# Optimization experiments

Measured on AMD Instinct MI355X. Metric: run time of the kernel, lower is better.

## Reference

```python
import jax, jax.numpy as jnp
import numpy as np

NUM_ITERATIONS = 3
SOFTMAX_DIM = 1  # softmax over out_capsules


def _squash(x, axis=-1):
    # scale = ||x|| / (1 + ||x||^2)  (leftthomas/CapsuleLayer squash)
    norm = jnp.linalg.norm(x, axis=axis, keepdims=True)
    return x * (norm / (1.0 + norm * norm))


def _normalize(x, axis=-1, eps=1e-12):
    n = jnp.linalg.norm(x, axis=axis, keepdims=True)
    return x / jnp.maximum(n, eps)


def setup_inputs() -> dict:
    key = jax.random.key(0)
    k1, k2, k3 = jax.random.split(key, 3)
    B, I, O, LIN, LOUT = 64, 512, 64, 8, 16
    x = jax.random.normal(k1, (B, I, LIN), dtype=jnp.float32)
    # xavier-uniform over last two dims of the 4D weight
    limit = float(np.sqrt(6.0 / (LIN + LOUT)))
    weight = jax.random.uniform(k2, (O, I, LOUT, LIN), jnp.float32, -limit, limit)
    blim = float(np.sqrt(6.0 / (O + LOUT)))
    bias = jax.random.uniform(k3, (O, LOUT), jnp.float32, -blim, blim)
    return {"x": x, "weight": weight, "bias": bias}


def reference(x, weight, bias):
    # priors[b,o,i,v] = sum_l weight[o,i,v,l] * x[b,i,l]  -> [B, O, I, Lout]
    priors = jnp.einsum('oivl,bil->boiv', weight, x)
    # k-means routing, 'dot' similarity
    out = jnp.mean(priors, axis=-2, keepdims=True)  # [B, O, 1, Lout]
    for _ in range(NUM_ITERATIONS):
        logits = jnp.sum(priors * _normalize(out, axis=-1), axis=-1, keepdims=True)  # [B,O,I,1]
        probs = jax.nn.softmax(logits, axis=SOFTMAX_DIM)  # over out_capsules
        out = jnp.sum(probs * priors, axis=-2, keepdims=True)  # [B,O,1,Lout]
    out = _squash(out, axis=-1).squeeze(-2)  # [B, O, Lout]
    return out + bias
```

## Files before the change

kernel.cpp:

```cpp
#include <hip/hip_runtime.h>
#include <hip/hip_bf16.h>
#include <cstdint>


typedef float float4v __attribute__((ext_vector_type(4)));
typedef float float2v __attribute__((ext_vector_type(2)));
typedef unsigned short ushort8 __attribute__((ext_vector_type(8)));

__device__ __forceinline__ float bf2f(unsigned short u) {
    union { unsigned int ui; float f; } cv;
    cv.ui = ((unsigned int)u) << 16;
    return cv.f;
}
__device__ __forceinline__ unsigned short f2bf(float f) {
    union { float f; unsigned int ui; } cv;
    cv.f = f;
    unsigned int u = cv.ui;
    unsigned int r = u + 0x7FFFu + ((u >> 16) & 1u);
    return (unsigned short)(r >> 16);
}

__global__ __launch_bounds__(256) void k_priors(const float* __restrict__ W,
                                                const float* __restrict__ x,
                                                unsigned short* __restrict__ priors,
                                                float* __restrict__ outb) {
    const int i = blockIdx.x;
    const int t = threadIdx.x;
    __shared__ float Wl[16 * 132];
    __shared__ float xl[512];

    {
        int j = (blockIdx.x * 256 + t) * 2;
        *(float2v*)(outb + j) = (float2v){0.0f, 0.0f};
    }

    if (t < 128) {
        float4v v = *(const float4v*)(x + ((size_t)(t >> 1) * 512 + i) * 8 + (size_t)(t & 1) * 4);
        *(float4v*)(xl + t * 4) = v;
    }

    const int r  = t & 15;
    const int bq = t >> 4;

    for (int oc = 0; oc < 4; ++oc) {
        __syncthreads();
        #pragma unroll
        for (int k = 0; k < 2; ++k) {
            int j  = t + k * 256;
            int ol = j >> 5;
            int r4 = j & 31;
            float4v v = *(const float4v*)(W + ((size_t)((oc * 16 + ol) * 512 + i)) * 128 + (size_t)r4 * 4);
            *(float4v*)(Wl + ol * 132 + r4 * 4) = v;
        }
        __syncthreads();

        float4v wreg[32];
        const float4v* wp = (const float4v*)(Wl + r * 132);
        #pragma unroll
        for (int j = 0; j < 32; ++j) wreg[j] = wp[j];

        const int o = oc * 16 + r;
        #pragma unroll
        for (int k = 0; k < 4; ++k) {
            const int b = bq + 16 * k;
            float4v xr0 = ((const float4v*)(xl + b * 8))[0];
            float4v xr1 = ((const float4v*)(xl + b * 8))[1];
            ushort8 u0, u1;
            #pragma unroll
            for (int v = 0; v < 16; ++v) {
                float s = 0.0f;
                #pragma unroll
                for (int l = 0; l < 8; ++l) {
                    int idx = v * 8 + l;
                    float wv = wreg[idx >> 2][idx & 3];
                    float xv = (l < 4) ? xr0[l & 3] : xr1[l & 3];
                    s = fmaf(wv, xv, s);
                }
                unsigned short hb = f2bf(s);
                if (v < 8) u0[v] = hb; else u1[v - 8] = hb;
            }
            unsigned short* dst = priors + ((size_t)(b * 512 + i) * 64 + o) * 16;
            *(ushort8*)(dst) = u0;
            *(ushort8*)(dst + 8) = u1;
        }
    }
}

__global__ __launch_bounds__(256) void k_sum0(const unsigned short* __restrict__ priors,
                                              float* __restrict__ out0) {
    const int b    = blockIdx.x >> 3;
    const int ic   = blockIdx.x & 7;
    const int t    = threadIdx.x;
    const int slot = t & 127;
    const int io   = t >> 7;
    const int o    = slot >> 1;
    const int vh   = slot & 1;

    float acc[8];
    #pragma unroll
    for (int j = 0; j < 8; ++j) acc[j] = 0.0f;

    const unsigned short* base = priors + (size_t)b * 524288 + (size_t)o * 16 + vh * 8;
    for (int k = 0; k < 32; ++k) {
        const int i = ic * 64 + k * 2 + io;
        ushort8 u = *(const ushort8*)(base + (size_t)i * 1024);
        #pragma unroll
        for (int j = 0; j < 8; ++j) acc[j] += bf2f(u[j]);
    }

    __shared__ float red[8 * 128];
    if (io == 1) {
        #pragma unroll
        for (int j = 0; j < 8; ++j) red[j * 128 + slot] = acc[j];
    }
    __syncthreads();
    if (io == 0) {
        float* dst = out0 + (size_t)b * 1024 + o * 16 + vh * 8;
        #pragma unroll
        for (int j = 0; j < 8; ++j) atomicAdd(dst + j, acc[j] + red[j * 128 + slot]);
    }
}

__global__ __launch_bounds__(256) void k_route(const unsigned short* __restrict__ priors,
                                               const float* __restrict__ out_prev,
                                               float* __restrict__ out_next) {
    const int b    = blockIdx.x >> 3;
    const int h    = blockIdx.x & 7;
    const int t    = threadIdx.x;
    const int w    = t >> 6;
    const int lane = t & 63;

    __shared__ float noutT[16 * 64];
    __shared__ float accbuf[4 * 1088];

    if (t < 64) {
        const float* po = out_prev + (size_t)b * 1024 + t * 16;
        float vv[16]; float n2 = 0.0f;
        #pragma unroll
        for (int j = 0; j < 16; ++j) { vv[j] = po[j]; n2 += vv[j] * vv[j]; }
        float n = fmaxf(sqrtf(n2), 1e-12f);
        float inv = 1.0f / n;
        #pragma unroll
        for (int j = 0; j < 16; ++j) noutT[j * 64 + t] = vv[j] * inv;
    }
    __syncthreads();

    float nr[16];
    #pragma unroll
    for (int j = 0; j < 16; ++j) nr[j] = noutT[j * 64 + lane];

    float acc[16];
    #pragma unroll
    for (int j = 0; j < 16; ++j) acc[j] = 0.0f;

    const size_t base = (size_t)b * 524288 + (size_t)lane * 16;
    for (int k = 0; k < 16; ++k) {
        const int i = h * 64 + w + 4 * k;
        const ushort8* pp = (const ushort8*)(priors + base + (size_t)i * 1024);
        ushort8 u0 = pp[0], u1 = pp[1];
        float pf[16];
        #pragma unroll
        for (int j = 0; j < 8; ++j) { pf[j] = bf2f(u0[j]); pf[8 + j] = bf2f(u1[j]); }

        float logit = 0.0f;
        #pragma unroll
        for (int j = 0; j < 16; ++j) logit = fmaf(pf[j], nr[j], logit);

        float m = logit;
        #pragma unroll
        for (int d = 1; d < 64; d <<= 1) m = fmaxf(m, __shfl_xor(m, d));
        float e = __expf(logit - m);
        float s = e;
        #pragma unroll
        for (int d = 1; d < 64; d <<= 1) s += __shfl_xor(s, d);
        float p = e / s;

        #pragma unroll
        for (int j = 0; j < 16; ++j) acc[j] = fmaf(p, pf[j], acc[j]);
    }

    #pragma unroll
    for (int j = 0; j < 16; ++j) accbuf[w * 1088 + lane * 17 + j] = acc[j];
    __syncthreads();

    for (int j = t; j < 1024; j += 256) {
        const int o = j >> 4, v = j & 15;
        const int idx = o * 17 + v;
        float s = accbuf[idx] + accbuf[1088 + idx] + accbuf[2176 + idx] + accbuf[3264 + idx];
        atomicAdd(out_next + (size_t)b * 1024 + j, s);
    }
}

__global__ __launch_bounds__(64) void k_fin(const float* __restrict__ outl,
                                            const float* __restrict__ bias,
                                            float* __restrict__ out) {
    const int b = blockIdx.x;
    const int o = threadIdx.x;
    const float* p = outl + (size_t)b * 1024 + o * 16;
    float vv[16]; float n2 = 0.0f;
    #pragma unroll
    for (int j = 0; j < 16; ++j) { vv[j] = p[j]; n2 += vv[j] * vv[j]; }
    float n = sqrtf(n2);
    float scale = n / (1.0f + n2);
    float* q = out + (size_t)b * 1024 + o * 16;
    #pragma unroll
    for (int j = 0; j < 16; ++j) q[j] = vv[j] * scale + bias[o * 16 + j];
}

extern "C" void kernel_launch(void* const* d_in, const int* in_sizes, int n_in,
                              void* d_out, int out_size, void* d_ws, size_t ws_size,
                              hipStream_t stream) {
    const float* x    = (const float*)d_in[0];
    const float* W    = (const float*)d_in[1];
    const float* bias = (const float*)d_in[2];
    float* out = (float*)d_out;

    unsigned short* priors = (unsigned short*)d_ws;
    float* outb = (float*)((char*)d_ws + (size_t)64 * 512 * 64 * 16 * 2);

    k_priors<<<512, 256, 0, stream>>>(W, x, priors, outb);
    k_sum0  <<<512, 256, 0, stream>>>(priors, outb);
    k_route <<<512, 256, 0, stream>>>(priors, outb,               outb + 65536);
    k_route <<<512, 256, 0, stream>>>(priors, outb + 65536,       outb + 2 * 65536);
    k_route <<<512, 256, 0, stream>>>(priors, outb + 2 * 65536,   outb + 3 * 65536);
    k_fin   <<<64, 64, 0, stream>>>(outb + 3 * 65536, bias, out);
}
```

Baseline: 99.74 us.

## Fuse sum and routing iterations into one cooperative kernel with register-resident priors

Replaces the sum0, three route and finalize kernels with a single cooperative-launch kernel of 256 blocks x 512 threads. Each thread loads its slice of bf16 priors into registers once and reuses it across all routing iterations, separated by grid-wide syncs. This removes four launches and three re-reads of the 64 MB priors buffer. In exchange it adds grid barrier cost and heavy register pressure (256 bytes of cached priors per thread), with a fallback to the old kernels if the cooperative launch fails.

```diff
diff --git a/kernel.cpp b/kernel.cpp
--- a/kernel.cpp
+++ b/kernel.cpp
@@ -1,5 +1,6 @@
 #include <hip/hip_runtime.h>
 #include <hip/hip_bf16.h>
+#include <hip/hip_cooperative_groups.h>
 #include <cstdint>
 
 
@@ -86,6 +87,137 @@
     }
 }
 
+__global__ __launch_bounds__(512, 2) void k_fused(const unsigned short* __restrict__ priors,
+                                                  float* __restrict__ outb,
+                                                  const float* __restrict__ bias,
+                                                  float* __restrict__ out) {
+    const int b    = blockIdx.x >> 2;
+    const int q    = blockIdx.x & 3;
+    const int t    = threadIdx.x;
+    const int w    = t >> 6;
+    const int lane = t & 63;
+
+    __shared__ float noutT[16 * 64];
+    __shared__ float red[7 * 1088];
+
+    ushort8 c0[16], c1[16];
+    float acc[16];
+    #pragma unroll
+    for (int j = 0; j < 16; ++j) acc[j] = 0.0f;
+
+    const unsigned short* basep = priors + (size_t)b * 524288
+                                + (size_t)(q * 128 + w * 16) * 1024 + (size_t)lane * 16;
+    #pragma unroll
+    for (int k = 0; k < 16; ++k) {
+        c0[k] = *(const ushort8*)(basep + (size_t)k * 1024);
+        c1[k] = *(const ushort8*)(basep + (size_t)k * 1024 + 8);
+        #pragma unroll
+        for (int j = 0; j < 8; ++j) {
+            acc[j]     += bf2f(c0[k][j]);
+            acc[8 + j] += bf2f(c1[k][j]);
+        }
+    }
+    if (w > 0) {
+        #pragma unroll
+        for (int j = 0; j < 16; ++j) red[(w - 1) * 1088 + lane * 17 + j] = acc[j];
+    }
+    __syncthreads();
+    if (w == 0) {
+        float* dst = outb + (size_t)b * 1024 + lane * 16;
+        #pragma unroll
+        for (int j = 0; j < 16; ++j) {
+            float s = acc[j];
+            #pragma unroll
+            for (int ww = 0; ww < 7; ++ww) s += red[ww * 1088 + lane * 17 + j];
+            atomicAdd(dst + j, s);
+        }
+    }
+
+    cooperative_groups::this_grid().sync();
+
+    for (int r = 0; r < 3; ++r) {
+        const float* oprev = outb + (size_t)r * 65536 + (size_t)b * 1024;
+        float*       onext = outb + (size_t)(r + 1) * 65536 + (size_t)b * 1024;
+
+        if (t < 64) {
+            float vv[16]; float n2 = 0.0f;
+            #pragma unroll
+            for (int j = 0; j < 16; ++j) {
+                vv[j] = __hip_atomic_load(oprev + t * 16 + j, __ATOMIC_RELAXED,
+                                          __HIP_MEMORY_SCOPE_AGENT);
+                n2 += vv[j] * vv[j];
+            }
+            float inv = 1.0f / fmaxf(sqrtf(n2), 1e-12f);
+            #pragma unroll
+            for (int j = 0; j < 16; ++j) noutT[j * 64 + t] = vv[j] * inv;
+        }
+        __syncthreads();
+
+        float nr[16];
+        #pragma unroll
+        for (int j = 0; j < 16; ++j) nr[j] = noutT[j * 64 + lane];
+
+        float a2[16];
+        #pragma unroll
+        for (int j = 0; j < 16; ++j) a2[j] = 0.0f;
+
+        #pragma unroll
+        for (int k = 0; k < 16; ++k) {
+            float pf[16];
+            #pragma unroll
+            for (int j = 0; j < 8; ++j) { pf[j] = bf2f(c0[k][j]); pf[8 + j] = bf2f(c1[k][j]); }
+
+            float logit = 0.0f;
+            #pragma unroll
+            for (int j = 0; j < 16; ++j) logit = fmaf(pf[j], nr[j], logit);
+
+            float m = logit;
+            #pragma unroll
+            for (int d = 1; d < 64; d <<= 1) m = fmaxf(m, __shfl_xor(m, d));
+            float e = __expf(logit - m);
+            float s = e;
+            #pragma unroll
+            for (int d = 1; d < 64; d <<= 1) s += __shfl_xor(s, d);
+            float p = e / s;
+
+            #pragma unroll
+            for (int j = 0; j < 16; ++j) a2[j] = fmaf(p, pf[j], a2[j]);
+        }
+
+        __syncthreads();
+        if (w > 0) {
+            #pragma unroll
+            for (int j = 0; j < 16; ++j) red[(w - 1) * 1088 + lane * 17 + j] = a2[j];
+        }
+        __syncthreads();
+        if (w == 0) {
+            #pragma unroll
+            for (int j = 0; j < 16; ++j) {
+                float s = a2[j];
+                #pragma unroll
+                for (int ww = 0; ww < 7; ++ww) s += red[ww * 1088 + lane * 17 + j];
+                atomicAdd(onext + lane * 16 + j, s);
+            }
+        }
+        cooperative_groups::this_grid().sync();
+    }
+
+    if (q == 0 && t < 64) {
+        const float* p = outb + (size_t)3 * 65536 + (size_t)b * 1024 + t * 16;
+        float vv[16]; float n2 = 0.0f;
+        #pragma unroll
+        for (int j = 0; j < 16; ++j) {
+            vv[j] = __hip_atomic_load(p + j, __ATOMIC_RELAXED, __HIP_MEMORY_SCOPE_AGENT);
+            n2 += vv[j] * vv[j];
+        }
+        float n = sqrtf(n2);
+        float sc = n / (1.0f + n2);
+        float* qd = out + (size_t)b * 1024 + t * 16;
+        #pragma unroll
+        for (int j = 0; j < 16; ++j) qd[j] = vv[j] * sc + bias[t * 16 + j];
+    }
+}
+
 __global__ __launch_bounds__(256) void k_sum0(const unsigned short* __restrict__ priors,
                                               float* __restrict__ out0) {
     const int b    = blockIdx.x >> 3;
@@ -138,8 +270,7 @@
         float vv[16]; float n2 = 0.0f;
         #pragma unroll
         for (int j = 0; j < 16; ++j) { vv[j] = po[j]; n2 += vv[j] * vv[j]; }
-        float n = fmaxf(sqrtf(n2), 1e-12f);
-        float inv = 1.0f / n;
+        float inv = 1.0f / fmaxf(sqrtf(n2), 1e-12f);
         #pragma unroll
         for (int j = 0; j < 16; ++j) noutT[j * 64 + t] = vv[j] * inv;
     }
@@ -219,9 +350,16 @@
     float* outb = (float*)((char*)d_ws + (size_t)64 * 512 * 64 * 16 * 2);
 
     k_priors<<<512, 256, 0, stream>>>(W, x, priors, outb);
-    k_sum0  <<<512, 256, 0, stream>>>(priors, outb);
-    k_route <<<512, 256, 0, stream>>>(priors, outb,               outb + 65536);
-    k_route <<<512, 256, 0, stream>>>(priors, outb + 65536,       outb + 2 * 65536);
-    k_route <<<512, 256, 0, stream>>>(priors, outb + 2 * 65536,   outb + 3 * 65536);
-    k_fin   <<<64, 64, 0, stream>>>(outb + 3 * 65536, bias, out);
-}
+
+    void* args[] = { (void*)&priors, (void*)&outb, (void*)&bias, (void*)&out };
+    hipError_t err = hipLaunchCooperativeKernel((const void*)k_fused, dim3(256), dim3(512),
+                                                args, 0, stream);
+    if (err != hipSuccess) {
+        (void)hipGetLastError();
+        k_sum0  <<<512, 256, 0, stream>>>(priors, outb);
+        k_route <<<512, 256, 0, stream>>>(priors, outb,               outb + 65536);
+        k_route <<<512, 256, 0, stream>>>(priors, outb + 65536,       outb + 2 * 65536);
+        k_route <<<512, 256, 0, stream>>>(priors, outb + 2 * 65536,   outb + 3 * 65536);
+        k_fin   <<<64, 64, 0, stream>>>(outb + 3 * 65536, bias, out);
+    }
+}
```

Measured after the change: 276.5 us. +177.2%, slower.

## Replace atomic accumulation with per-chunk partial buffers and double grid size

Applied to the files above, without the earlier changes.

The routing and sum kernels now write per-chunk partial sums into a [B,16,1024] buffer instead of doing float atomicAdds into a shared output. The consumer kernels (next route step and final squash) reduce the 16 partials themselves. Each kernel launch also doubles its block count, with each block covering half as many input capsules, to raise parallelism. This removes the atomics and the zero-initialisation done inside k_priors, at the cost of extra partial-buffer traffic and a redundant 16-way reduction in every block.

```diff
diff --git a/kernel.cpp b/kernel.cpp
--- a/kernel.cpp
+++ b/kernel.cpp
@@ -4,7 +4,6 @@
 
 
 typedef float float4v __attribute__((ext_vector_type(4)));
-typedef float float2v __attribute__((ext_vector_type(2)));
 typedef unsigned short ushort8 __attribute__((ext_vector_type(8)));
 
 __device__ __forceinline__ float bf2f(unsigned short u) {
@@ -22,17 +21,11 @@
 
 __global__ __launch_bounds__(256) void k_priors(const float* __restrict__ W,
                                                 const float* __restrict__ x,
-                                                unsigned short* __restrict__ priors,
-                                                float* __restrict__ outb) {
+                                                unsigned short* __restrict__ priors) {
     const int i = blockIdx.x;
     const int t = threadIdx.x;
     __shared__ float Wl[16 * 132];
     __shared__ float xl[512];
-
-    {
-        int j = (blockIdx.x * 256 + t) * 2;
-        *(float2v*)(outb + j) = (float2v){0.0f, 0.0f};
-    }
 
     if (t < 128) {
         float4v v = *(const float4v*)(x + ((size_t)(t >> 1) * 512 + i) * 8 + (size_t)(t & 1) * 4);
@@ -87,9 +80,9 @@
 }
 
 __global__ __launch_bounds__(256) void k_sum0(const unsigned short* __restrict__ priors,
-                                              float* __restrict__ out0) {
-    const int b    = blockIdx.x >> 3;
-    const int ic   = blockIdx.x & 7;
+                                              float* __restrict__ part0) {
+    const int b    = blockIdx.x >> 4;
+    const int ic   = blockIdx.x & 15;
     const int t    = threadIdx.x;
     const int slot = t & 127;
     const int io   = t >> 7;
@@ -101,8 +94,9 @@
     for (int j = 0; j < 8; ++j) acc[j] = 0.0f;
 
     const unsigned short* base = priors + (size_t)b * 524288 + (size_t)o * 16 + vh * 8;
-    for (int k = 0; k < 32; ++k) {
-        const int i = ic * 64 + k * 2 + io;
+    #pragma unroll
+    for (int k = 0; k < 16; ++k) {
+        const int i = ic * 32 + k * 2 + io;
         ushort8 u = *(const ushort8*)(base + (size_t)i * 1024);
         #pragma unroll
         for (int j = 0; j < 8; ++j) acc[j] += bf2f(u[j]);
@@ -115,17 +109,17 @@
     }
     __syncthreads();
     if (io == 0) {
-        float* dst = out0 + (size_t)b * 1024 + o * 16 + vh * 8;
-        #pragma unroll
-        for (int j = 0; j < 8; ++j) atomicAdd(dst + j, acc[j] + red[j * 128 + slot]);
+        float* dst = part0 + (size_t)b * 16384 + (size_t)ic * 1024 + o * 16 + vh * 8;
+        #pragma unroll
+        for (int j = 0; j < 8; ++j) dst[j] = acc[j] + red[j * 128 + slot];
     }
 }
 
 __global__ __launch_bounds__(256) void k_route(const unsigned short* __restrict__ priors,
-                                               const float* __restrict__ out_prev,
-                                               float* __restrict__ out_next) {
-    const int b    = blockIdx.x >> 3;
-    const int h    = blockIdx.x & 7;
+                                               const float* __restrict__ part_prev,
+                                               float* __restrict__ part_next) {
+    const int b    = blockIdx.x >> 4;
+    const int h    = blockIdx.x & 15;
     const int t    = threadIdx.x;
     const int w    = t >> 6;
     const int lane = t & 63;
@@ -134,12 +128,20 @@
     __shared__ float accbuf[4 * 1088];
 
     if (t < 64) {
-        const float* po = out_prev + (size_t)b * 1024 + t * 16;
+        const float* pp = part_prev + (size_t)b * 16384 + t * 16;
+        float4v s4[4];
+        #pragma unroll
+        for (int g = 0; g < 4; ++g) s4[g] = (float4v){0.f, 0.f, 0.f, 0.f};
+        #pragma unroll
+        for (int ic = 0; ic < 16; ++ic) {
+            #pragma unroll
+            for (int g = 0; g < 4; ++g)
+                s4[g] += *(const float4v*)(pp + (size_t)ic * 1024 + g * 4);
+        }
         float vv[16]; float n2 = 0.0f;
         #pragma unroll
-        for (int j = 0; j < 16; ++j) { vv[j] = po[j]; n2 += vv[j] * vv[j]; }
-        float n = fmaxf(sqrtf(n2), 1e-12f);
-        float inv = 1.0f / n;
+        for (int j = 0; j < 16; ++j) { vv[j] = s4[j >> 2][j & 3]; n2 += vv[j] * vv[j]; }
+        float inv = 1.0f / fmaxf(sqrtf(n2), 1e-12f);
         #pragma unroll
         for (int j = 0; j < 16; ++j) noutT[j * 64 + t] = vv[j] * inv;
     }
@@ -154,8 +156,9 @@
     for (int j = 0; j < 16; ++j) acc[j] = 0.0f;
 
     const size_t base = (size_t)b * 524288 + (size_t)lane * 16;
-    for (int k = 0; k < 16; ++k) {
-        const int i = h * 64 + w + 4 * k;
+    #pragma unroll
+    for (int k = 0; k < 8; ++k) {
+        const int i = h * 32 + w + 4 * k;
         const ushort8* pp = (const ushort8*)(priors + base + (size_t)i * 1024);
         ushort8 u0 = pp[0], u1 = pp[1];
         float pf[16];
@@ -183,23 +186,32 @@
     for (int j = 0; j < 16; ++j) accbuf[w * 1088 + lane * 17 + j] = acc[j];
     __syncthreads();
 
+    float* dst = part_next + (size_t)b * 16384 + (size_t)h * 1024;
     for (int j = t; j < 1024; j += 256) {
         const int o = j >> 4, v = j & 15;
         const int idx = o * 17 + v;
-        float s = accbuf[idx] + accbuf[1088 + idx] + accbuf[2176 + idx] + accbuf[3264 + idx];
-        atomicAdd(out_next + (size_t)b * 1024 + j, s);
-    }
-}
-
-__global__ __launch_bounds__(64) void k_fin(const float* __restrict__ outl,
+        dst[j] = accbuf[idx] + accbuf[1088 + idx] + accbuf[2176 + idx] + accbuf[3264 + idx];
+    }
+}
+
+__global__ __launch_bounds__(64) void k_fin(const float* __restrict__ part3,
                                             const float* __restrict__ bias,
                                             float* __restrict__ out) {
     const int b = blockIdx.x;
     const int o = threadIdx.x;
-    const float* p = outl + (size_t)b * 1024 + o * 16;
+    const float* pp = part3 + (size_t)b * 16384 + o * 16;
+    float4v s4[4];
+    #pragma unroll
+    for (int g = 0; g < 4; ++g) s4[g] = (float4v){0.f, 0.f, 0.f, 0.f};
+    #pragma unroll
+    for (int ic = 0; ic < 16; ++ic) {
+        #pragma unroll
+        for (int g = 0; g < 4; ++g)
+            s4[g] += *(const float4v*)(pp + (size_t)ic * 1024 + g * 4);
+    }
     float vv[16]; float n2 = 0.0f;
     #pragma unroll
-    for (int j = 0; j < 16; ++j) { vv[j] = p[j]; n2 += vv[j] * vv[j]; }
+    for (int j = 0; j < 16; ++j) { vv[j] = s4[j >> 2][j & 3]; n2 += vv[j] * vv[j]; }
     float n = sqrtf(n2);
     float scale = n / (1.0f + n2);
     float* q = out + (size_t)b * 1024 + o * 16;
@@ -216,12 +228,16 @@
     float* out = (float*)d_out;
 
     unsigned short* priors = (unsigned short*)d_ws;
-    float* outb = (float*)((char*)d_ws + (size_t)64 * 512 * 64 * 16 * 2);
-
-    k_priors<<<512, 256, 0, stream>>>(W, x, priors, outb);
-    k_sum0  <<<512, 256, 0, stream>>>(priors, outb);
-    k_route <<<512, 256, 0, stream>>>(priors, outb,               outb + 65536);
-    k_route <<<512, 256, 0, stream>>>(priors, outb + 65536,       outb + 2 * 65536);
-    k_route <<<512, 256, 0, stream>>>(priors, outb + 2 * 65536,   outb + 3 * 65536);
-    k_fin   <<<64, 64, 0, stream>>>(outb + 3 * 65536, bias, out);
-}
+    float* part = (float*)((char*)d_ws + (size_t)64 * 512 * 64 * 16 * 2);
+    float* part0 = part;
+    float* part1 = part + 1048576;
+    float* part2 = part + 2 * 1048576;
+    float* part3 = part + 3 * 1048576;
+
+    k_priors<<<512, 256, 0, stream>>>(W, x, priors);
+    k_sum0  <<<1024, 256, 0, stream>>>(priors, part0);
+    k_route <<<1024, 256, 0, stream>>>(priors, part0, part1);
+    k_route <<<1024, 256, 0, stream>>>(priors, part1, part2);
+    k_route <<<1024, 256, 0, stream>>>(priors, part2, part3);
+    k_fin   <<<64, 64, 0, stream>>>(part3, bias, out);
+}
```

Result: slower. 106.0 us (+6.2%).
